# Kernel optimization log

Measured on AMD Instinct MI355X. Metric: run time of the kernel, lower is better.

## Reference

```python
import jax, jax.numpy as jnp
import numpy as np

N, F_IN, C0, C1, H, E, G = 50000, 128, 64, 64, 4, 800000, 256
NEG_SLOPE = 0.2
BN_EPS = 1e-5


def setup_inputs() -> dict:
    key = jax.random.key(0)
    ks = jax.random.split(key, 16)
    d = {
        'x': jax.random.normal(ks[0], (N, F_IN), dtype=jnp.float32),
        'edge_index': jax.random.randint(ks[1], (2, E), 0, N, dtype=jnp.int64),
        'batch': jnp.sort(jax.random.randint(ks[2], (N,), 0, G, dtype=jnp.int64)),
        # conv1 params
        'W1': jax.random.normal(ks[3], (F_IN, H * C0), dtype=jnp.float32) * (1.0 / np.sqrt(F_IN)),
        'att_src1': jax.random.normal(ks[4], (H, C0), dtype=jnp.float32) * 0.1,
        'att_dst1': jax.random.normal(ks[5], (H, C0), dtype=jnp.float32) * 0.1,
        'b1': jnp.zeros((H * C0,), dtype=jnp.float32),
        # batchnorm params
        'gamma': jnp.ones((H * C0,), dtype=jnp.float32),
        'beta': jnp.zeros((H * C0,), dtype=jnp.float32),
        # conv2 params
        'W2': jax.random.normal(ks[6], (H * C0, H * C1), dtype=jnp.float32) * (1.0 / np.sqrt(H * C0)),
        'att_src2': jax.random.normal(ks[7], (H, C1), dtype=jnp.float32) * 0.1,
        'att_dst2': jax.random.normal(ks[8], (H, C1), dtype=jnp.float32) * 0.1,
        'b2': jnp.zeros((H * C1,), dtype=jnp.float32),
    }
    return d


def _gat_layer(x, W, a_src, a_dst, b, src, dst, heads, ch):
    # x: [N, Fin] -> h: [N, H, C]
    h = (x @ W).reshape(N, heads, ch)
    al_src = jnp.sum(h * a_src, axis=-1)  # [N, H]
    al_dst = jnp.sum(h * a_dst, axis=-1)  # [N, H]
    e = jax.nn.leaky_relu(al_src[src] + al_dst[dst], NEG_SLOPE)  # [E', H]
    m = jax.ops.segment_max(e, dst, num_segments=N)
    m = jnp.where(jnp.isfinite(m), m, 0.0)
    ex = jnp.exp(e - m[dst])
    denom = jax.ops.segment_sum(ex, dst, num_segments=N)
    alpha = ex / (denom[dst] + 1e-16)  # softmax over in-neighborhood of dst
    out = jax.ops.segment_sum(alpha[:, :, None] * h[src], dst, num_segments=N)  # [N, H, C]
    return out.reshape(N, heads * ch) + b


def _batchnorm(x, gamma, beta):
    mu = jnp.mean(x, axis=0)
    var = jnp.var(x, axis=0)
    return gamma * (x - mu) / jnp.sqrt(var + BN_EPS) + beta


def reference(x, edge_index, batch, W1, att_src1, att_dst1, b1, gamma, beta,
              W2, att_src2, att_dst2, b2):
    # add self loops (PyG GATConv default)
    loops = jnp.arange(N, dtype=edge_index.dtype)
    src = jnp.concatenate([edge_index[0], loops])
    dst = jnp.concatenate([edge_index[1], loops])

    x1 = _gat_layer(x, W1, att_src1, att_dst1, b1, src, dst, H, C0)
    x1 = jax.nn.relu(_batchnorm(x1, gamma, beta))
    x2 = jax.nn.relu(_gat_layer(x1, W2, att_src2, att_dst2, b2, src, dst, H, C1))

    xc = jnp.concatenate([x1, x2], axis=1)  # [N, H*C0 + H*C1]
    counts = jax.ops.segment_sum(jnp.ones((N,), xc.dtype), batch, num_segments=G)
    x_mean = jax.ops.segment_sum(xc, batch, num_segments=G) / jnp.maximum(counts, 1.0)[:, None]
    x_max = jax.ops.segment_max(xc, batch, num_segments=G)
    x_max = jnp.where(jnp.isfinite(x_max), x_max, 0.0)
    return jnp.concatenate([x_mean, x_max], axis=1)  # [G, 2*(H*C0+H*C1)]
```

## Files before the change

kernel.cpp:

```cpp
#include <hip/hip_runtime.h>
#include <hip/hip_bf16.h>
#include <math.h>

#define NN 50000
#define FIN 128
#define FH 256
#define NE 800000
#define NG 256
#define ELLS 64
#define NEG_SLOPE 0.2f
#define BN_EPS 1e-5f

typedef short bf16x8 __attribute__((ext_vector_type(8)));
typedef unsigned short u16x8 __attribute__((ext_vector_type(8)));
typedef unsigned long long u64x2 __attribute__((ext_vector_type(2)));
typedef float f32x4 __attribute__((ext_vector_type(4)));

__device__ __forceinline__ float lrelu(float x) { return x > 0.f ? x : NEG_SLOPE * x; }
__device__ __forceinline__ float bf2f(unsigned short u) { return __uint_as_float(((unsigned int)u) << 16); }
__device__ __forceinline__ unsigned short f2bf(float f) {
    __hip_bfloat16 b = __float2bfloat16(f);
    return *reinterpret_cast<unsigned short*>(&b);
}

__global__ __launch_bounds__(256) void k_prep(const float* __restrict__ W1, unsigned short* __restrict__ W1t,
                                              const float* __restrict__ W2, unsigned short* __restrict__ W2t,
                                              int* __restrict__ cnt, int* __restrict__ colIdx) {
    int bid = blockIdx.x;
    if (bid < 384) {
        int o = bid * 256 + threadIdx.x;
        if (o < 256 * 128) {
            int c = o >> 7, k = o & 127;
            W1t[o] = f2bf(W1[(size_t)k * 256 + c]);
        } else {
            o -= 256 * 128;
            if (o < 256 * 256) {
                int c = o >> 8, k = o & 255;
                W2t[o] = f2bf(W2[(size_t)k * 256 + c]);
            }
        }
    } else {
        int i = (bid - 384) * 256 + threadIdx.x;
        if (i < NN) {
            cnt[i] = 1;
            colIdx[(size_t)i * ELLS] = i;
        }
    }
}

template<int MODE>
__global__ __launch_bounds__(256) void k_gemm(const float* __restrict__ Af, const unsigned short* __restrict__ Ab,
                                              const unsigned short* __restrict__ Bt,
                                              unsigned short* __restrict__ C,
                                              const float* __restrict__ attS, const float* __restrict__ attD,
                                              float* __restrict__ alsrc, float* __restrict__ aldst,
                                              const float* __restrict__ bnsum, const float* __restrict__ bnsq,
                                              const float* __restrict__ gamma, const float* __restrict__ beta,
                                              const int* __restrict__ eiFill, int* __restrict__ cntFill,
                                              int* __restrict__ colIdxFill, int nGemm,
                                              int M, int K) {
    __shared__ short As[128 * 40];
    __shared__ short Bs[128 * 40];
    __shared__ float s_scale[256], s_shift[256];
    int bid = blockIdx.x;
    if (MODE == 0 && bid >= nGemm) {
        int i = (bid - nGemm) * 256 + threadIdx.x;
        if (i < NE) {
            int s = eiFill[i], d = eiFill[NE + i];
            int pos = atomicAdd(&cntFill[d], 1);
            if (pos < ELLS) colIdxFill[(size_t)d * ELLS + pos] = s;
        }
        return;
    }
    int tid = threadIdx.x;
    int lane = tid & 63, wid = tid >> 6;
    int wr = wid >> 1, wc = wid & 1;
    int row0 = (bid >> 1) * 128, col0 = (bid & 1) * 128;
    if (MODE == 1) {
        const float invN = 1.f / (float)NN;
        float mean = bnsum[tid] * invN;
        float var  = bnsq[tid] * invN - mean * mean;
        float istd = rsqrtf(var + BN_EPS);
        float sc = gamma[tid] * istd;
        s_scale[tid] = sc;
        s_shift[tid] = beta[tid] - mean * sc;
        __syncthreads();
    }
    f32x4 acc[4][4];
#pragma unroll
    for (int m = 0; m < 4; ++m)
#pragma unroll
        for (int n = 0; n < 4; ++n) acc[m][n] = (f32x4){0.f, 0.f, 0.f, 0.f};

    int r = tid >> 2, seg = tid & 3;
    int koff = (lane >> 4) * 8;

    for (int k0 = 0; k0 < K; k0 += 32) {
#pragma unroll
        for (int j = 0; j < 2; ++j) {
            int row = r + j * 64;
            int grow = row0 + row;
            bf16x8 va;
            if (MODE == 0) {
                float4 v0 = make_float4(0.f, 0.f, 0.f, 0.f), v1 = v0;
                if (grow < M) {
                    const float* ap = Af + (size_t)grow * K + k0 + seg * 8;
                    v0 = *(const float4*)ap;
                    v1 = *((const float4*)ap + 1);
                }
                va[0] = (short)f2bf(v0.x); va[1] = (short)f2bf(v0.y);
                va[2] = (short)f2bf(v0.z); va[3] = (short)f2bf(v0.w);
                va[4] = (short)f2bf(v1.x); va[5] = (short)f2bf(v1.y);
                va[6] = (short)f2bf(v1.z); va[7] = (short)f2bf(v1.w);
            } else {
                bf16x8 raw = {0, 0, 0, 0, 0, 0, 0, 0};
                if (grow < M) raw = *(const bf16x8*)(Ab + (size_t)grow * K + k0 + seg * 8);
                int cb = k0 + seg * 8;
#pragma unroll
                for (int k = 0; k < 8; ++k) {
                    float f = bf2f((unsigned short)raw[k]) * s_scale[cb + k] + s_shift[cb + k];
                    va[k] = (short)f2bf(fmaxf(f, 0.f));
                }
            }
            *(bf16x8*)&As[row * 40 + seg * 8] = va;
            bf16x8 vb = *(const bf16x8*)(Bt + (size_t)(col0 + row) * K + k0 + seg * 8);
            *(bf16x8*)&Bs[row * 40 + seg * 8] = vb;
        }
        __syncthreads();
        bf16x8 af[4], bfr[4];
#pragma unroll
        for (int m = 0; m < 4; ++m)
            af[m] = *(const bf16x8*)&As[(wr * 64 + m * 16 + (lane & 15)) * 40 + koff];
#pragma unroll
        for (int n = 0; n < 4; ++n)
            bfr[n] = *(const bf16x8*)&Bs[(wc * 64 + n * 16 + (lane & 15)) * 40 + koff];
#pragma unroll
        for (int m = 0; m < 4; ++m)
#pragma unroll
            for (int n = 0; n < 4; ++n)
                acc[m][n] = __builtin_amdgcn_mfma_f32_16x16x32_bf16(af[m], bfr[n], acc[m][n], 0, 0, 0);
        __syncthreads();
    }
#pragma unroll
    for (int m = 0; m < 4; ++m) {
        int rbase = row0 + wr * 64 + m * 16 + (lane >> 4) * 4;
#pragma unroll
        for (int j = 0; j < 4; ++j) {
            int row = rbase + j;
            if (row < M) {
#pragma unroll
                for (int n = 0; n < 4; ++n) {
                    int col = col0 + wc * 64 + n * 16 + (lane & 15);
                    C[(size_t)row * 256 + col] = f2bf(acc[m][n][j]);
                }
            }
        }
    }
    float ps[4][4], pd[4][4];
#pragma unroll
    for (int m = 0; m < 4; ++m)
#pragma unroll
        for (int j = 0; j < 4; ++j) { ps[m][j] = 0.f; pd[m][j] = 0.f; }
#pragma unroll
    for (int n = 0; n < 4; ++n) {
        int col = col0 + wc * 64 + n * 16 + (lane & 15);
        float aS = attS[col], aD = attD[col];
#pragma unroll
        for (int m = 0; m < 4; ++m)
#pragma unroll
            for (int j = 0; j < 4; ++j) {
                ps[m][j] = fmaf(acc[m][n][j], aS, ps[m][j]);
                pd[m][j] = fmaf(acc[m][n][j], aD, pd[m][j]);
            }
    }
#pragma unroll
    for (int off = 1; off < 16; off <<= 1) {
#pragma unroll
        for (int m = 0; m < 4; ++m)
#pragma unroll
            for (int j = 0; j < 4; ++j) {
                ps[m][j] += __shfl_xor(ps[m][j], off);
                pd[m][j] += __shfl_xor(pd[m][j], off);
            }
    }
    if ((lane & 15) == 0) {
        int head = (col0 >> 6) + wc;
#pragma unroll
        for (int m = 0; m < 4; ++m) {
            int rbase = row0 + wr * 64 + m * 16 + (lane >> 4) * 4;
#pragma unroll
            for (int j = 0; j < 4; ++j) {
                int row = rbase + j;
                if (row < M) {
                    alsrc[row * 4 + head] = ps[m][j];
                    aldst[row * 4 + head] = pd[m][j];
                }
            }
        }
    }
}

__global__ __launch_bounds__(256) void k_gat_agg(const int* __restrict__ cnt, const int* __restrict__ colIdx,
    const float* __restrict__ alsrc, const float* __restrict__ aldst, const unsigned short* __restrict__ h,
    const float* __restrict__ bias, unsigned short* __restrict__ outb, int relu_nt, int n) {
    __shared__ float ex_s[4][2][32][4];
    __shared__ int   src_s[4][2][32];
    int wave = threadIdx.x >> 6, lane = threadIdx.x & 63;
    int half = lane >> 5, hlane = lane & 31;
    int node = blockIdx.x * 8 + wave * 2 + half;
    int deg = min(cnt[node], ELLS);
    const int* crow = colIdx + (size_t)node * ELLS;
    int hf = hlane >> 3;
    float4 ad = *(const float4*)(aldst + (size_t)node * 4);
    float m0 = -1e30f, m1 = -1e30f, m2 = -1e30f, m3 = -1e30f;
    float d0 = 0.f, d1 = 0.f, d2 = 0.f, d3 = 0.f;
    float acc[8];
#pragma unroll
    for (int k = 0; k < 8; ++k) acc[k] = 0.f;

    for (int base = 0; base < deg; base += 32) {
        int cnt32 = min(32, deg - base);
        int src = node;
        float e0 = -1e30f, e1 = -1e30f, e2 = -1e30f, e3 = -1e30f;
        if (hlane < cnt32) {
            src = crow[base + hlane];
            float4 as = *(const float4*)(alsrc + (size_t)src * 4);
            e0 = lrelu(as.x + ad.x);
            e1 = lrelu(as.y + ad.y);
            e2 = lrelu(as.z + ad.z);
            e3 = lrelu(as.w + ad.w);
        }
        float c0 = e0, c1 = e1, c2 = e2, c3 = e3;
#pragma unroll
        for (int off = 16; off > 0; off >>= 1) {
            c0 = fmaxf(c0, __shfl_xor(c0, off));
            c1 = fmaxf(c1, __shfl_xor(c1, off));
            c2 = fmaxf(c2, __shfl_xor(c2, off));
            c3 = fmaxf(c3, __shfl_xor(c3, off));
        }
        float nm0 = fmaxf(m0, c0), nm1 = fmaxf(m1, c1), nm2 = fmaxf(m2, c2), nm3 = fmaxf(m3, c3);
        float sc0 = __expf(m0 - nm0), sc1 = __expf(m1 - nm1), sc2 = __expf(m2 - nm2), sc3 = __expf(m3 - nm3);
        float x0 = __expf(e0 - nm0), x1 = __expf(e1 - nm1), x2 = __expf(e2 - nm2), x3 = __expf(e3 - nm3);
        float s0 = x0, s1 = x1, s2 = x2, s3 = x3;
#pragma unroll
        for (int off = 16; off > 0; off >>= 1) {
            s0 += __shfl_xor(s0, off);
            s1 += __shfl_xor(s1, off);
            s2 += __shfl_xor(s2, off);
            s3 += __shfl_xor(s3, off);
        }
        d0 = d0 * sc0 + s0; d1 = d1 * sc1 + s1; d2 = d2 * sc2 + s2; d3 = d3 * sc3 + s3;
        m0 = nm0; m1 = nm1; m2 = nm2; m3 = nm3;
        float scl = (hf == 0) ? sc0 : (hf == 1) ? sc1 : (hf == 2) ? sc2 : sc3;
#pragma unroll
        for (int k = 0; k < 8; ++k) acc[k] *= scl;
        ex_s[wave][half][hlane][0] = x0; ex_s[wave][half][hlane][1] = x1;
        ex_s[wave][half][hlane][2] = x2; ex_s[wave][half][hlane][3] = x3;
        src_s[wave][half][hlane] = src;
        for (int j = 0; j < cnt32; j += 2) {
            float w0 = ex_s[wave][half][j][hf];
            bf16x8 h0 = *(const bf16x8*)(h + (size_t)src_s[wave][half][j] * 256 + hlane * 8);
            float w1 = 0.f;
            bf16x8 h1 = {0, 0, 0, 0, 0, 0, 0, 0};
            if (j + 1 < cnt32) {
                w1 = ex_s[wave][half][j + 1][hf];
                h1 = *(const bf16x8*)(h + (size_t)src_s[wave][half][j + 1] * 256 + hlane * 8);
            }
#pragma unroll
            for (int k = 0; k < 8; ++k)
                acc[k] = fmaf(w0, bf2f((unsigned short)h0[k]), acc[k]);
#pragma unroll
            for (int k = 0; k < 8; ++k)
                acc[k] = fmaf(w1, bf2f((unsigned short)h1[k]), acc[k]);
        }
    }

    float dd = (hf == 0) ? d0 : (hf == 1) ? d1 : (hf == 2) ? d2 : d3;
    float inv = 1.f / (dd + 1e-16f);
    float4 b0 = *(const float4*)(bias + hlane * 8);
    float4 b1 = *(const float4*)(bias + hlane * 8 + 4);
    float o[8];
    o[0] = acc[0] * inv + b0.x; o[1] = acc[1] * inv + b0.y;
    o[2] = acc[2] * inv + b0.z; o[3] = acc[3] * inv + b0.w;
    o[4] = acc[4] * inv + b1.x; o[5] = acc[5] * inv + b1.y;
    o[6] = acc[6] * inv + b1.z; o[7] = acc[7] * inv + b1.w;
    u16x8 ob;
    if (relu_nt) {
#pragma unroll
        for (int k = 0; k < 8; ++k) ob[k] = f2bf(fmaxf(o[k], 0.f));
        u64x2 w = *(u64x2*)&ob;
        __builtin_nontemporal_store(w, (u64x2*)(outb + (size_t)node * 256 + hlane * 8));
    } else {
#pragma unroll
        for (int k = 0; k < 8; ++k) ob[k] = f2bf(o[k]);
        *(u64x2*)(outb + (size_t)node * 256 + hlane * 8) = *(u64x2*)&ob;
    }
}

__global__ __launch_bounds__(256) void k_bn_stats(const unsigned short* __restrict__ xin, float* bnsum, float* bnsq) {
    int t = threadIdx.x;
    int r0 = blockIdx.x * 250;
    float s = 0.f, q = 0.f;
    for (int r = r0; r < r0 + 250; ++r) {
        float v = bf2f(xin[(size_t)r * 256 + t]);
        s += v; q += v * v;
    }
    atomicAdd(&bnsum[t], s);
    atomicAdd(&bnsq[t], q);
}

__global__ __launch_bounds__(512) void k_pool(const unsigned short* __restrict__ x1pre,
    const unsigned short* __restrict__ x2b, const int* __restrict__ batch,
    const float* __restrict__ bnsum, const float* __restrict__ bnsq,
    const float* __restrict__ gamma, const float* __restrict__ beta,
    float* __restrict__ out) {
    int g = blockIdx.x;
    __shared__ int sLo, sHi;
    if (threadIdx.x == 0) {
        int lo = 0, hi = NN;
        while (lo < hi) { int m = (lo + hi) >> 1; if (batch[m] < g) lo = m + 1; else hi = m; }
        sLo = lo;
    }
    if (threadIdx.x == 1) {
        int lo = 0, hi = NN;
        while (lo < hi) { int m = (lo + hi) >> 1; if (batch[m] < g + 1) lo = m + 1; else hi = m; }
        sHi = lo;
    }
    __syncthreads();
    int lo = sLo, hi = sHi, cnt = hi - lo;
    int t = threadIdx.x;
    bool first = t < 256;
    int f = first ? t : t - 256;
    const unsigned short* src = first ? x1pre : x2b;
    float sc = 1.f, sh = 0.f;
    if (first) {
        const float invN = 1.f / (float)NN;
        float mean = bnsum[f] * invN;
        float var  = bnsq[f] * invN - mean * mean;
        float istd = rsqrtf(var + BN_EPS);
        sc = gamma[f] * istd;
        sh = beta[f] - mean * sc;
    }
    float s = 0.f, mx = 0.f;
    int r = lo;
    for (; r + 1 < hi; r += 2) {
        float va = bf2f(src[(size_t)r * 256 + f]);
        float vb = bf2f(src[(size_t)(r + 1) * 256 + f]);
        if (first) {
            va = fmaxf(va * sc + sh, 0.f);
            vb = fmaxf(vb * sc + sh, 0.f);
        }
        s += va + vb;
        mx = fmaxf(mx, fmaxf(va, vb));
    }
    if (r < hi) {
        float va = bf2f(src[(size_t)r * 256 + f]);
        if (first) va = fmaxf(va * sc + sh, 0.f);
        s += va; mx = fmaxf(mx, va);
    }
    float mean = (cnt > 0) ? s / (float)cnt : 0.f;
    int off = first ? 0 : 256;
    out[g * 1024 + off + f] = mean;
    out[g * 1024 + 512 + off + f] = mx;
}

extern "C" void kernel_launch(void* const* d_in, const int* in_sizes, int n_in,
                              void* d_out, int out_size, void* d_ws, size_t ws_size,
                              hipStream_t stream) {
    const float* x     = (const float*)d_in[0];
    const int*   ei    = (const int*)d_in[1];
    const int*   batch = (const int*)d_in[2];
    const float* W1    = (const float*)d_in[3];
    const float* asrc1 = (const float*)d_in[4];
    const float* adst1 = (const float*)d_in[5];
    const float* b1    = (const float*)d_in[6];
    const float* gamma = (const float*)d_in[7];
    const float* beta  = (const float*)d_in[8];
    const float* W2    = (const float*)d_in[9];
    const float* asrc2 = (const float*)d_in[10];
    const float* adst2 = (const float*)d_in[11];
    const float* b2    = (const float*)d_in[12];
    float* out = (float*)d_out;

    char* p = (char*)d_ws;
    auto alloc = [&](size_t bytes) -> void* {
        void* r = (void*)p;
        p += (bytes + 255) & ~(size_t)255;
        return r;
    };
    unsigned short* hb    = (unsigned short*)alloc((size_t)NN * 256 * 2);
    unsigned short* x1pre = (unsigned short*)alloc((size_t)NN * 256 * 2);
    unsigned short* x2b   = (unsigned short*)alloc((size_t)NN * 256 * 2);
    unsigned short* W1t   = (unsigned short*)alloc((size_t)256 * 128 * 2);
    unsigned short* W2t   = (unsigned short*)alloc((size_t)256 * 256 * 2);
    float* alsrc = (float*)alloc((size_t)NN * 4 * 4);
    float* aldst = (float*)alloc((size_t)NN * 4 * 4);
    float* bnsum = (float*)alloc(256 * 4);
    float* bnsq  = (float*)alloc(256 * 4);
    int*   cnt   = (int*)alloc((size_t)NN * 4);
    int*   colIdx = (int*)alloc((size_t)NN * ELLS * 4);

    (void)hipMemsetAsync(bnsum, 0, 2 * 1024, stream);

    const int nbE = (NE + 255) / 256;
    const int nGemm = 2 * ((NN + 127) / 128);

    k_prep<<<384 + 196, 256, 0, stream>>>(W1, W1t, W2, W2t, cnt, colIdx);

    k_gemm<0><<<nGemm + nbE, 256, 0, stream>>>(x, nullptr, W1t, hb, asrc1, adst1, alsrc, aldst,
                                               nullptr, nullptr, nullptr, nullptr,
                                               ei, cnt, colIdx, nGemm, NN, 128);
    k_gat_agg<<<NN / 8, 256, 0, stream>>>(cnt, colIdx, alsrc, aldst, hb, b1, x1pre, 0, NN);
    k_bn_stats<<<200, 256, 0, stream>>>(x1pre, bnsum, bnsq);

    k_gemm<1><<<nGemm, 256, 0, stream>>>(nullptr, x1pre, W2t, hb, asrc2, adst2, alsrc, aldst,
                                         bnsum, bnsq, gamma, beta,
                                         nullptr, nullptr, nullptr, nGemm, NN, 256);
    k_gat_agg<<<NN / 8, 256, 0, stream>>>(cnt, colIdx, alsrc, aldst, hb, b2, x2b, 1, NN);

    k_pool<<<NG, 512, 0, stream>>>(x1pre, x2b, batch, bnsum, bnsq, gamma, beta, out);
}
```

Measured before the change: 293.9 us.

## Prefetch next GEMM K-tile into registers and stage epilogue through LDS

The GEMM kernel now loads the next K-slice of A and B into registers while the MFMA work for the current slice runs, so global-load latency overlaps with compute. The epilogue writes the accumulator tile into LDS in two halves and then stores C with coalesced 16-byte rows instead of scattered 2-byte writes. The attention logits are recomputed from the bf16-rounded values in LDS, with the attention vectors cached in shared memory. This costs more registers and adds barriers, and the logits now come from bf16-rounded h rather than fp32 accumulators.

```diff
diff --git a/kernel.cpp b/kernel.cpp
--- a/kernel.cpp
+++ b/kernel.cpp
@@ -59,9 +59,13 @@
                                               const int* __restrict__ eiFill, int* __restrict__ cntFill,
                                               int* __restrict__ colIdxFill, int nGemm,
                                               int M, int K) {
-    __shared__ short As[128 * 40];
-    __shared__ short Bs[128 * 40];
-    __shared__ float s_scale[256], s_shift[256];
+    __shared__ short lds[10240];
+    __shared__ float sAs_[128], sAd_[128];
+    __shared__ float s_scale[MODE == 1 ? 256 : 1];
+    __shared__ float s_shift[MODE == 1 ? 256 : 1];
+    short* As = lds;
+    short* Bs = lds + 5120;
+
     int bid = blockIdx.x;
     if (MODE == 0 && bid >= nGemm) {
         int i = (bid - nGemm) * 256 + threadIdx.x;
@@ -76,6 +80,11 @@
     int lane = tid & 63, wid = tid >> 6;
     int wr = wid >> 1, wc = wid & 1;
     int row0 = (bid >> 1) * 128, col0 = (bid & 1) * 128;
+
+    if (tid < 128) {
+        sAs_[tid] = attS[col0 + tid];
+        sAd_[tid] = attD[col0 + tid];
+    }
     if (MODE == 1) {
         const float invN = 1.f / (float)NN;
         float mean = bnsum[tid] * invN;
@@ -95,38 +104,66 @@
     int r = tid >> 2, seg = tid & 3;
     int koff = (lane >> 4) * 8;
 
+    float4 qa0[2], qa1[2];
+    bf16x8 qab[2];
+    bf16x8 qb[2];
+    const float4 zf4 = make_float4(0.f, 0.f, 0.f, 0.f);
+    const bf16x8 zb8 = {0, 0, 0, 0, 0, 0, 0, 0};
+
+#pragma unroll
+    for (int j = 0; j < 2; ++j) {
+        int grow = row0 + r + j * 64;
+        if (MODE == 0) {
+            if (grow < M) {
+                const float* ap = Af + (size_t)grow * K + seg * 8;
+                qa0[j] = *(const float4*)ap;
+                qa1[j] = *((const float4*)ap + 1);
+            } else { qa0[j] = zf4; qa1[j] = zf4; }
+        } else {
+            qab[j] = (grow < M) ? *(const bf16x8*)(Ab + (size_t)grow * K + seg * 8) : zb8;
+        }
+        qb[j] = *(const bf16x8*)(Bt + (size_t)(col0 + r + j * 64) * K + seg * 8);
+    }
+
     for (int k0 = 0; k0 < K; k0 += 32) {
 #pragma unroll
         for (int j = 0; j < 2; ++j) {
             int row = r + j * 64;
-            int grow = row0 + row;
             bf16x8 va;
             if (MODE == 0) {
-                float4 v0 = make_float4(0.f, 0.f, 0.f, 0.f), v1 = v0;
-                if (grow < M) {
-                    const float* ap = Af + (size_t)grow * K + k0 + seg * 8;
-                    v0 = *(const float4*)ap;
-                    v1 = *((const float4*)ap + 1);
-                }
-                va[0] = (short)f2bf(v0.x); va[1] = (short)f2bf(v0.y);
-                va[2] = (short)f2bf(v0.z); va[3] = (short)f2bf(v0.w);
-                va[4] = (short)f2bf(v1.x); va[5] = (short)f2bf(v1.y);
-                va[6] = (short)f2bf(v1.z); va[7] = (short)f2bf(v1.w);
+                va[0] = (short)f2bf(qa0[j].x); va[1] = (short)f2bf(qa0[j].y);
+                va[2] = (short)f2bf(qa0[j].z); va[3] = (short)f2bf(qa0[j].w);
+                va[4] = (short)f2bf(qa1[j].x); va[5] = (short)f2bf(qa1[j].y);
+                va[6] = (short)f2bf(qa1[j].z); va[7] = (short)f2bf(qa1[j].w);
             } else {
-                bf16x8 raw = {0, 0, 0, 0, 0, 0, 0, 0};
-                if (grow < M) raw = *(const bf16x8*)(Ab + (size_t)grow * K + k0 + seg * 8);
                 int cb = k0 + seg * 8;
 #pragma unroll
                 for (int k = 0; k < 8; ++k) {
-                    float f = bf2f((unsigned short)raw[k]) * s_scale[cb + k] + s_shift[cb + k];
+                    float f = bf2f((unsigned short)qab[j][k]) * s_scale[cb + k] + s_shift[cb + k];
                     va[k] = (short)f2bf(fmaxf(f, 0.f));
                 }
             }
             *(bf16x8*)&As[row * 40 + seg * 8] = va;
-            bf16x8 vb = *(const bf16x8*)(Bt + (size_t)(col0 + row) * K + k0 + seg * 8);
-            *(bf16x8*)&Bs[row * 40 + seg * 8] = vb;
+            *(bf16x8*)&Bs[row * 40 + seg * 8] = qb[j];
         }
         __syncthreads();
+        int kn = k0 + 32;
+        if (kn < K) {
+#pragma unroll
+            for (int j = 0; j < 2; ++j) {
+                int grow = row0 + r + j * 64;
+                if (MODE == 0) {
+                    if (grow < M) {
+                        const float* ap = Af + (size_t)grow * K + kn + seg * 8;
+                        qa0[j] = *(const float4*)ap;
+                        qa1[j] = *((const float4*)ap + 1);
+                    } else { qa0[j] = zf4; qa1[j] = zf4; }
+                } else {
+                    qab[j] = (grow < M) ? *(const bf16x8*)(Ab + (size_t)grow * K + kn + seg * 8) : zb8;
+                }
+                qb[j] = *(const bf16x8*)(Bt + (size_t)(col0 + r + j * 64) * K + kn + seg * 8);
+            }
+        }
         bf16x8 af[4], bfr[4];
 #pragma unroll
         for (int m = 0; m < 4; ++m)
@@ -141,62 +178,58 @@
                 acc[m][n] = __builtin_amdgcn_mfma_f32_16x16x32_bf16(af[m], bfr[n], acc[m][n], 0, 0, 0);
         __syncthreads();
     }
-#pragma unroll
-    for (int m = 0; m < 4; ++m) {
-        int rbase = row0 + wr * 64 + m * 16 + (lane >> 4) * 4;
-#pragma unroll
-        for (int j = 0; j < 4; ++j) {
-            int row = rbase + j;
-            if (row < M) {
+
+    const int CST = 138;
+#pragma unroll 1
+    for (int hh = 0; hh < 2; ++hh) {
+        if (wr == hh) {
+#pragma unroll
+            for (int m = 0; m < 4; ++m) {
+                int rl = m * 16 + (lane >> 4) * 4;
 #pragma unroll
                 for (int n = 0; n < 4; ++n) {
-                    int col = col0 + wc * 64 + n * 16 + (lane & 15);
-                    C[(size_t)row * 256 + col] = f2bf(acc[m][n][j]);
+                    int cl = wc * 64 + n * 16 + (lane & 15);
+#pragma unroll
+                    for (int j = 0; j < 4; ++j)
+                        lds[(rl + j) * CST + cl] = (short)f2bf(acc[m][n][j]);
                 }
             }
         }
-    }
-    float ps[4][4], pd[4][4];
-#pragma unroll
-    for (int m = 0; m < 4; ++m)
-#pragma unroll
-        for (int j = 0; j < 4; ++j) { ps[m][j] = 0.f; pd[m][j] = 0.f; }
-#pragma unroll
-    for (int n = 0; n < 4; ++n) {
-        int col = col0 + wc * 64 + n * 16 + (lane & 15);
-        float aS = attS[col], aD = attD[col];
-#pragma unroll
-        for (int m = 0; m < 4; ++m)
-#pragma unroll
-            for (int j = 0; j < 4; ++j) {
-                ps[m][j] = fmaf(acc[m][n][j], aS, ps[m][j]);
-                pd[m][j] = fmaf(acc[m][n][j], aD, pd[m][j]);
-            }
-    }
-#pragma unroll
-    for (int off = 1; off < 16; off <<= 1) {
-#pragma unroll
-        for (int m = 0; m < 4; ++m)
-#pragma unroll
-            for (int j = 0; j < 4; ++j) {
-                ps[m][j] += __shfl_xor(ps[m][j], off);
-                pd[m][j] += __shfl_xor(pd[m][j], off);
-            }
-    }
-    if ((lane & 15) == 0) {
-        int head = (col0 >> 6) + wc;
-#pragma unroll
-        for (int m = 0; m < 4; ++m) {
-            int rbase = row0 + wr * 64 + m * 16 + (lane >> 4) * 4;
-#pragma unroll
-            for (int j = 0; j < 4; ++j) {
-                int row = rbase + j;
-                if (row < M) {
-                    alsrc[row * 4 + head] = ps[m][j];
-                    aldst[row * 4 + head] = pd[m][j];
-                }
-            }
-        }
+        __syncthreads();
+        int rl = tid >> 2, q = tid & 3;
+        int grow = row0 + hh * 64 + rl;
+        if (grow < M) {
+            const short* cp = &lds[rl * CST + q * 32];
+            bf16x8 v0 = *(const bf16x8*)(cp + 0);
+            bf16x8 v1 = *(const bf16x8*)(cp + 8);
+            bf16x8 v2 = *(const bf16x8*)(cp + 16);
+            bf16x8 v3 = *(const bf16x8*)(cp + 24);
+            unsigned short* op = C + (size_t)grow * 256 + col0 + q * 32;
+            *(bf16x8*)(op + 0)  = v0;
+            *(bf16x8*)(op + 8)  = v1;
+            *(bf16x8*)(op + 16) = v2;
+            *(bf16x8*)(op + 24) = v3;
+            float ps = 0.f, pd = 0.f;
+            const float* aS = &sAs_[q * 32];
+            const float* aD = &sAd_[q * 32];
+#pragma unroll
+            for (int k = 0; k < 8; ++k) {
+                float f0 = bf2f((unsigned short)v0[k]);
+                float f1 = bf2f((unsigned short)v1[k]);
+                float f2 = bf2f((unsigned short)v2[k]);
+                float f3 = bf2f((unsigned short)v3[k]);
+                ps += f0 * aS[k] + f1 * aS[k + 8] + f2 * aS[k + 16] + f3 * aS[k + 24];
+                pd += f0 * aD[k] + f1 * aD[k + 8] + f2 * aD[k + 16] + f3 * aD[k + 24];
+            }
+            ps += __shfl_xor(ps, 1);
+            pd += __shfl_xor(pd, 1);
+            if ((q & 1) == 0) {
+                int head = (col0 >> 6) + (q >> 1);
+                alsrc[grow * 4 + head] = ps;
+                aldst[grow * 4 + head] = pd;
+            }
+        }
+        __syncthreads();
     }
 }
 
```

Measured after the change: 293.3 us. About the same (-0.2%).
